# Optimization experiments

Hardware: AMD Instinct MI355X
Metric: run time of the kernel (lower is better)

Reference implementation:

```python
import jax, jax.numpy as jnp
import numpy as np

B = 65536
IN_F = 1024
OUT_F = 1024
N_ACT = 4  # len(activation_functions): tanh, sin, relu, sigmoid (cyclic over columns)


def setup_inputs() -> dict:
    key = jax.random.key(0)
    k1, k2 = jax.random.split(key)
    x = jax.random.normal(k1, (B, IN_F), dtype=jnp.float32)
    # xavier_uniform for weight [out, in]
    limit = float(np.sqrt(6.0 / (IN_F + OUT_F)))
    W = jax.random.uniform(k2, (OUT_F, IN_F), dtype=jnp.float32, minval=-limit, maxval=limit)
    b = jnp.zeros((OUT_F,), dtype=jnp.float32)
    return {"input": x, "W": W, "b": b}


def _apply_cyclic_acts(y):
    # column i gets activation (i % N_ACT); OUT_F % N_ACT == 0 so reshape to groups
    Bb, O = y.shape
    yg = y.reshape(Bb, O // N_ACT, N_ACT)
    out = jnp.stack([
        jnp.tanh(yg[..., 0]),
        jnp.sin(yg[..., 1]),
        jax.nn.relu(yg[..., 2]),
        jax.nn.sigmoid(yg[..., 3]),
    ], axis=-1)
    return out.reshape(Bb, O)


def reference(input, W, b) -> jnp.ndarray:
    y = jnp.einsum('bi,oi->bo', input, W) + b  # F.linear
    return _apply_cyclic_acts(y)
```

## Files before the change

### kernel.cpp

```cpp
#include <hip/hip_runtime.h>

constexpr int B_ROWS = 65536;
constexpr int IN_F   = 1024;
constexpr int OUT_F  = 1024;

constexpr int BDIM = 256;
constexpr int BM = 128, BN = 128, BK = 32;

typedef __bf16 bf16x8 __attribute__((ext_vector_type(8)));
typedef float  f32x4  __attribute__((ext_vector_type(4)));

__device__ __forceinline__ bf16x8 cvt8(f32x4 u0, f32x4 u1) {
    bf16x8 v;
    v[0] = (__bf16)u0[0]; v[1] = (__bf16)u0[1]; v[2] = (__bf16)u0[2]; v[3] = (__bf16)u0[3];
    v[4] = (__bf16)u1[0]; v[5] = (__bf16)u1[1]; v[6] = (__bf16)u1[2]; v[7] = (__bf16)u1[3];
    return v;
}

#define LDS_SYNC() asm volatile("s_waitcnt lgkmcnt(0)\n\ts_barrier" ::: "memory")

__global__ __launch_bounds__(BDIM, 2)
void fused_linear_act(const float* __restrict__ X,
                      const float* __restrict__ W,
                      const float* __restrict__ bias,
                      float* __restrict__ O)
{
    __shared__ __attribute__((aligned(16))) unsigned char lds[2 * 16384];

    const int bx  = blockIdx.x;
    const int xcd = bx & 7;
    const int idx = bx >> 3;
    const int nt  = idx & 7;
    const int mt  = xcd + 8 * (idx >> 3);
    const int m0 = mt * BM;
    const int n0 = nt * BN;

    const int tid  = threadIdx.x;
    const int lane = tid & 63;
    const int wave = tid >> 6;
    const int wm = (wave >> 1) * 64;
    const int wn = (wave & 1) * 64;
    const int lrow = lane & 15;
    const int quad = lane >> 4;

    const int srow = tid >> 2;
    const int sseg = tid & 3;

    f32x4 acc[4][4];
    #pragma unroll
    for (int i = 0; i < 4; ++i)
        #pragma unroll
        for (int j = 0; j < 4; ++j)
            acc[i][j] = (f32x4){0.f, 0.f, 0.f, 0.f};

    const float* xa = X + (size_t)(m0 + srow) * IN_F + sseg * 8;
    const float* xb = xa + (size_t)64 * IN_F;
    const float* wa = W + (size_t)(n0 + srow) * IN_F + sseg * 8;
    const float* wb = wa + (size_t)64 * IN_F;

    unsigned char* wr = &lds[((srow >> 4) * 64 + sseg * 16 + (srow & 15)) * 16];
    const unsigned char* rdA = &lds[(wm >> 4) * 1024 + lane * 16];
    const unsigned char* rdB = &lds[8192 + (wn >> 4) * 1024 + lane * 16];

    f32x4 A00, A01, A10, A11, B00, B01, B10, B11;
    A00 = *(const f32x4*)(xa);     A01 = *(const f32x4*)(xa + 4);
    A10 = *(const f32x4*)(xb);     A11 = *(const f32x4*)(xb + 4);
    B00 = *(const f32x4*)(wa);     B01 = *(const f32x4*)(wa + 4);
    B10 = *(const f32x4*)(wb);     B11 = *(const f32x4*)(wb + 4);
    int koff = 0;

    auto stage = [&](int buf) {
        unsigned char* w = wr + buf * 16384;
        *(bf16x8*)(w +     0) = cvt8(A00, A01);
        *(bf16x8*)(w +  4096) = cvt8(A10, A11);
        *(bf16x8*)(w +  8192) = cvt8(B00, B01);
        *(bf16x8*)(w + 12288) = cvt8(B10, B11);
        koff = (koff + BK) & (IN_F - 1);
        A00 = *(const f32x4*)(xa + koff); A01 = *(const f32x4*)(xa + koff + 4);
        A10 = *(const f32x4*)(xb + koff); A11 = *(const f32x4*)(xb + koff + 4);
        B00 = *(const f32x4*)(wa + koff); B01 = *(const f32x4*)(wa + koff + 4);
        B10 = *(const f32x4*)(wb + koff); B11 = *(const f32x4*)(wb + koff + 4);
    };

    auto compute = [&](int buf) {
        const unsigned char* ra = rdA + buf * 16384;
        const unsigned char* rb = rdB + buf * 16384;
        bf16x8 af[4], bfr[4];
        #pragma unroll
        for (int t = 0; t < 4; ++t) af[t]  = *(const bf16x8*)(ra + t * 1024);
        #pragma unroll
        for (int t = 0; t < 4; ++t) bfr[t] = *(const bf16x8*)(rb + t * 1024);
        #pragma unroll
        for (int i = 0; i < 4; ++i)
            #pragma unroll
            for (int j = 0; j < 4; ++j)
                acc[i][j] = __builtin_amdgcn_mfma_f32_16x16x32_bf16(af[i], bfr[j], acc[i][j], 0, 0, 0);
    };

    #pragma unroll 1
    for (int it = 0; it < IN_F / BK; it += 2) {
        stage(0);
        LDS_SYNC();
        compute(0);
        stage(1);
        LDS_SYNC();
        compute(1);
    }

    const int s = lane & 3;
    const float kmul = (s == 0) ? -2.f : -1.f;
    const float aa   = (s == 0) ?  2.f :  1.f;
    const float cc   = (s == 0) ? -1.f :  0.f;
    const bool  is_sin  = (s == 1);
    const bool  is_relu = (s == 2);

    #pragma unroll
    for (int j = 0; j < 4; ++j) {
        const int gc = n0 + wn + j * 16 + lrow;
        const float bv = bias[gc];
        #pragma unroll
        for (int i = 0; i < 4; ++i) {
            const int gr0 = m0 + wm + i * 16 + quad * 4;
            float* op = O + (size_t)gr0 * OUT_F + gc;
            #pragma unroll
            for (int r = 0; r < 4; ++r) {
                const float y = acc[i][j][r] + bv;
                const float e = __expf(kmul * y);
                const float g = fmaf(aa, __builtin_amdgcn_rcpf(1.f + e), cc);
                const float sv = __sinf(y);
                const float rv = fmaxf(y, 0.f);
                const float res = is_sin ? sv : (is_relu ? rv : g);
                op[(size_t)r * OUT_F] = res;
            }
        }
    }
}

extern "C" void kernel_launch(void* const* d_in, const int* in_sizes, int n_in,
                              void* d_out, int out_size, void* d_ws, size_t ws_size,
                              hipStream_t stream) {
    const float* X = (const float*)d_in[0];
    const float* W = (const float*)d_in[1];
    const float* b = (const float*)d_in[2];
    float* O = (float*)d_out;

    const int grid = (B_ROWS / BM) * (OUT_F / BN);
    fused_linear_act<<<grid, BDIM, 0, stream>>>(X, W, b, O);
}
```

Baseline: 637.4 us.

## Pre-convert W to bf16 and stream it via global_load_lds

A small pre-kernel converts W to bf16 in workspace each call. The main kernel then loads W tiles directly into LDS with global_load_lds, with one-stage lookahead and vmcnt-based barriers, while X is still staged through registers. Launch bounds rise to 4 blocks per CU. This is meant to cut W global traffic and conversion work, and free registers for higher occupancy. The cost is an extra kernel launch, plus correctness that depends on the vmcnt counting and the LDS layout.

```diff
diff --git a/kernel.cpp b/kernel.cpp
--- a/kernel.cpp
+++ b/kernel.cpp
@@ -17,11 +17,27 @@
     return v;
 }
 
-#define LDS_SYNC() asm volatile("s_waitcnt lgkmcnt(0)\n\ts_barrier" ::: "memory")
+__device__ __forceinline__ void glds16(const __bf16* g, unsigned char* l) {
+    __builtin_amdgcn_global_load_lds(
+        (const __attribute__((address_space(1))) unsigned int*)(const void*)g,
+        (__attribute__((address_space(3))) unsigned int*)(void*)l,
+        16, 0, 0);
+}
 
-__global__ __launch_bounds__(BDIM, 2)
+#define BAR_CNT() asm volatile("s_waitcnt vmcnt(4) lgkmcnt(0)\n\ts_barrier" ::: "memory")
+#define BAR_ALL() asm volatile("s_waitcnt vmcnt(0) lgkmcnt(0)\n\ts_barrier" ::: "memory")
+
+__global__ __launch_bounds__(256)
+void w_to_bf16(const float* __restrict__ W, __bf16* __restrict__ Wb) {
+    const int i = (blockIdx.x * 256 + threadIdx.x) * 8;
+    f32x4 a = *(const f32x4*)(W + i);
+    f32x4 b = *(const f32x4*)(W + i + 4);
+    *(bf16x8*)(Wb + i) = cvt8(a, b);
+}
+
+__global__ __launch_bounds__(BDIM, 4)
 void fused_linear_act(const float* __restrict__ X,
-                      const float* __restrict__ W,
+                      const __bf16* __restrict__ Wb,
                       const float* __restrict__ bias,
                       float* __restrict__ O)
 {
@@ -55,33 +71,41 @@
 
     const float* xa = X + (size_t)(m0 + srow) * IN_F + sseg * 8;
     const float* xb = xa + (size_t)64 * IN_F;
-    const float* wa = W + (size_t)(n0 + srow) * IN_F + sseg * 8;
-    const float* wb = wa + (size_t)64 * IN_F;
+
+    const __bf16* wsrc0 = Wb + (size_t)(n0 + 16 * wave + lrow) * IN_F + quad * 8;
+    const __bf16* wsrc1 = wsrc0 + (size_t)64 * IN_F;
+    unsigned char* ldsB0 = lds + 8192 + wave * 1024;
+    unsigned char* ldsB1 = ldsB0 + 4096;
 
     unsigned char* wr = &lds[((srow >> 4) * 64 + sseg * 16 + (srow & 15)) * 16];
     const unsigned char* rdA = &lds[(wm >> 4) * 1024 + lane * 16];
     const unsigned char* rdB = &lds[8192 + (wn >> 4) * 1024 + lane * 16];
 
-    f32x4 A00, A01, A10, A11, B00, B01, B10, B11;
-    A00 = *(const f32x4*)(xa);     A01 = *(const f32x4*)(xa + 4);
-    A10 = *(const f32x4*)(xb);     A11 = *(const f32x4*)(xb + 4);
-    B00 = *(const f32x4*)(wa);     B01 = *(const f32x4*)(wa + 4);
-    B10 = *(const f32x4*)(wb);     B11 = *(const f32x4*)(wb + 4);
-    int koff = 0;
+    f32x4 A00 = *(const f32x4*)(xa);
+    f32x4 A01 = *(const f32x4*)(xa + 4);
+    f32x4 A10 = *(const f32x4*)(xb);
+    f32x4 A11 = *(const f32x4*)(xb + 4);
+    glds16(wsrc0, ldsB0);
+    glds16(wsrc1, ldsB1);
+    __builtin_amdgcn_sched_barrier(0);
 
-    auto stage = [&](int buf) {
+    int koffA = 0;
+    int koffB = 0;
+
+    auto stageA = [&](int buf) {
         unsigned char* w = wr + buf * 16384;
-        *(bf16x8*)(w +     0) = cvt8(A00, A01);
-        *(bf16x8*)(w +  4096) = cvt8(A10, A11);
-        *(bf16x8*)(w +  8192) = cvt8(B00, B01);
-        *(bf16x8*)(w + 12288) = cvt8(B10, B11);
-        koff = (koff + BK) & (IN_F - 1);
-        A00 = *(const f32x4*)(xa + koff); A01 = *(const f32x4*)(xa + koff + 4);
-        A10 = *(const f32x4*)(xb + koff); A11 = *(const f32x4*)(xb + koff + 4);
-        B00 = *(const f32x4*)(wa + koff); B01 = *(const f32x4*)(wa + koff + 4);
-        B10 = *(const f32x4*)(wb + koff); B11 = *(const f32x4*)(wb + koff + 4);
+        *(bf16x8*)(w +    0) = cvt8(A00, A01);
+        *(bf16x8*)(w + 4096) = cvt8(A10, A11);
+        koffA = (koffA + BK) & (IN_F - 1);
+        A00 = *(const f32x4*)(xa + koffA); A01 = *(const f32x4*)(xa + koffA + 4);
+        A10 = *(const f32x4*)(xb + koffA); A11 = *(const f32x4*)(xb + koffA + 4);
     };
-
+    auto stageB = [&](int buf) {
+        koffB += BK;
+        glds16(wsrc0 + koffB, ldsB0 + buf * 16384);
+        glds16(wsrc1 + koffB, ldsB1 + buf * 16384);
+        __builtin_amdgcn_sched_barrier(0);
+    };
     auto compute = [&](int buf) {
         const unsigned char* ra = rdA + buf * 16384;
         const unsigned char* rb = rdB + buf * 16384;
@@ -98,14 +122,12 @@
     };
 
     #pragma unroll 1
-    for (int it = 0; it < IN_F / BK; it += 2) {
-        stage(0);
-        LDS_SYNC();
-        compute(0);
-        stage(1);
-        LDS_SYNC();
-        compute(1);
+    for (int it = 0; it < IN_F / BK - 2; it += 2) {
+        stageA(0); BAR_CNT(); stageB(1); compute(0);
+        stageA(1); BAR_CNT(); stageB(0); compute(1);
     }
+    stageA(0); BAR_CNT(); stageB(1); compute(0);
+    stageA(1); BAR_ALL(); compute(1);
 
     const int s = lane & 3;
     const float kmul = (s == 0) ? -2.f : -1.f;
@@ -143,7 +165,10 @@
     const float* W = (const float*)d_in[1];
     const float* b = (const float*)d_in[2];
     float* O = (float*)d_out;
+    __bf16* Wb = (__bf16*)d_ws;
+
+    w_to_bf16<<<(OUT_F * IN_F) / (256 * 8), 256, 0, stream>>>(W, Wb);
 
     const int grid = (B_ROWS / BM) * (OUT_F / BN);
-    fused_linear_act<<<grid, BDIM, 0, stream>>>(X, W, b, O);
+    fused_linear_act<<<grid, BDIM, 0, stream>>>(X, Wb, b, O);
 }
```

Measured after the change: 654.8 us. +2.7%, slower.
